# Kernel optimization log

Measured on AMD Instinct MI355X. Metric: run time of the kernel, lower is better.

## Reference

```python
import jax, jax.numpy as jnp
import numpy as np

B, D, R = 16384, 4096, 64       # batch tokens, embed_dim, low_rank_dimension
N_PART = 8                       # number of subspace partitions
P = R // N_PART                  # partition size = 8
N_SEL = 4                        # partitions selected per example


def setup_inputs() -> dict:
    key = jax.random.key(0)
    k1, k2, k3, k4 = jax.random.split(key, 4)
    base = jax.random.normal(k1, (B, D), dtype=jnp.float32)
    source = jax.random.normal(k2, (B, D), dtype=jnp.float32)
    # orthogonal low-rank rotation (torch.nn.utils.parametrizations.orthogonal)
    W, _ = jnp.linalg.qr(jax.random.normal(k3, (D, R), dtype=jnp.float32))  # [D, R], orthonormal cols
    subspaces = jax.random.randint(k4, (B, N_SEL), 0, N_PART)               # partition ids per example
    return {"base": base, "source": source, "W": W, "subspaces": subspaces}


def reference(base, source, W, subspaces):
    # rotate into low-rank space: [B, R]
    rotated_base = base @ W
    rotated_source = source @ W
    diff = rotated_source - rotated_base

    # per-example selected rotated-space indices (contiguous partitions of size P)
    # idx[b] = concat over selected partitions of [p*P, p*P+P)
    idx = (subspaces[:, :, None] * P + jnp.arange(P)).reshape(B, N_SEL * P)  # [B, N_SEL*P]

    # Selecting columns of diff and matching rows of W.T, then matmul, is
    # equivalent to masking unselected rotated dims to zero and doing one GEMM.
    mask = jnp.zeros((B, R), dtype=diff.dtype).at[jnp.arange(B)[:, None], idx].set(1.0)
    output = base + (diff * mask) @ W.T  # [B, D]
    return output.astype(base.dtype)
```

## Files before the change

### kernel.cpp

```cpp
#include <hip/hip_runtime.h>


#define D_DIM 4096
#define R_DIM 64
#define BM    16
#define KC    64
#define KW    1024

typedef short bf16vec8 __attribute__((ext_vector_type(8)));
typedef float f32x4v  __attribute__((ext_vector_type(4)));

#define OFF_STAGE   0
#define OFF_SCRATCH 8192
#define OFF_RM      26624
#define SMEM_BYTES  28672

__device__ __forceinline__ unsigned int f2bf_u(float f) {
  unsigned int u = __builtin_bit_cast(unsigned int, f);
  return (u + 0x7fffu + ((u >> 16) & 1u)) >> 16;
}
__device__ __forceinline__ unsigned int pack2bf(float a, float b) {
  return f2bf_u(a) | (f2bf_u(b) << 16);
}
__device__ __forceinline__ float bfbits2f(unsigned short s) {
  unsigned int u = ((unsigned int)s) << 16;
  return __builtin_bit_cast(float, u);
}

__global__ __launch_bounds__(256)
void lrri_prep(const float* __restrict__ W, unsigned short* __restrict__ Wt,
               unsigned short* __restrict__ Wb) {
  const int idx = blockIdx.x * blockDim.x + threadIdx.x;
  const int k = idx >> 4;
  const int j = (idx & 15) * 4;
  float4 w = *(const float4*)(W + (size_t)k * R_DIM + j);
  ushort4 p;
  p.x = (unsigned short)f2bf_u(w.x);
  p.y = (unsigned short)f2bf_u(w.y);
  p.z = (unsigned short)f2bf_u(w.z);
  p.w = (unsigned short)f2bf_u(w.w);
  *(ushort4*)(Wb + (size_t)k * R_DIM + j) = p;
  Wt[(size_t)(j + 0) * D_DIM + k] = p.x;
  Wt[(size_t)(j + 1) * D_DIM + k] = p.y;
  Wt[(size_t)(j + 2) * D_DIM + k] = p.z;
  Wt[(size_t)(j + 3) * D_DIM + k] = p.w;
}

template<bool USE_WS>
__global__ __launch_bounds__(256, 4)
void lrri_fused(const float* __restrict__ base, const float* __restrict__ srcp,
                const float* __restrict__ W, const int* __restrict__ subs,
                const unsigned short* __restrict__ Wt_bf,
                const unsigned short* __restrict__ Wb_bf,
                float* __restrict__ out)
{
  __shared__ __align__(16) unsigned char smem[SMEM_BYTES];
  const int tid  = threadIdx.x;
  const int wave = tid >> 6;
  const int lane = tid & 63;
  const int l4   = lane & 15;
  const int g    = lane >> 4;
  const long rowbase = (long)blockIdx.x * BM;

  unsigned short* stage = (unsigned short*)(smem + OFF_STAGE + wave * 2048);

  f32x4v acc[4];
  #pragma unroll
  for (int t = 0; t < 4; ++t) acc[t] = (f32x4v){0.f, 0.f, 0.f, 0.f};

  const int kw0 = wave * KW;
  #pragma unroll 1
  for (int c = 0; c < KW / KC; ++c) {
    const int kbase = kw0 + c * KC;
    float4 b4[4], s4[4];
    #pragma unroll
    for (int i = 0; i < 4; ++i) {
      const int r = g + i * 4;
      const long off = (rowbase + r) * D_DIM + kbase + l4 * 4;
      b4[i] = *(const float4*)(base + off);
      s4[i] = *(const float4*)(srcp + off);
    }
    #pragma unroll
    for (int i = 0; i < 4; ++i) {
      const int r = g + i * 4;
      uint2 dp;
      dp.x = pack2bf(s4[i].x - b4[i].x, s4[i].y - b4[i].y);
      dp.y = pack2bf(s4[i].z - b4[i].z, s4[i].w - b4[i].w);
      *(uint2*)((unsigned char*)stage + r * 128 + l4 * 8) = dp;
    }
    uint4 af[2];
    #pragma unroll
    for (int s = 0; s < 2; ++s)
      af[s] = *(const uint4*)((unsigned char*)stage + l4 * 128 + s * 64 + g * 16);
    #pragma unroll
    for (int t = 0; t < 4; ++t) {
      #pragma unroll
      for (int s = 0; s < 2; ++s) {
        uint4 bfrag;
        if (USE_WS) {
          bfrag = *(const uint4*)(Wt_bf + (size_t)(t * 16 + l4) * D_DIM +
                                  kbase + s * 32 + g * 8);
        } else {
          unsigned int p[4];
          #pragma unroll
          for (int e2 = 0; e2 < 4; ++e2) {
            float wa = W[(size_t)(kbase + s * 32 + g * 8 + e2 * 2    ) * R_DIM + t * 16 + l4];
            float wb = W[(size_t)(kbase + s * 32 + g * 8 + e2 * 2 + 1) * R_DIM + t * 16 + l4];
            p[e2] = pack2bf(wa, wb);
          }
          bfrag.x = p[0]; bfrag.y = p[1]; bfrag.z = p[2]; bfrag.w = p[3];
        }
        acc[t] = __builtin_amdgcn_mfma_f32_16x16x32_bf16(
            __builtin_bit_cast(bf16vec8, af[s]),
            __builtin_bit_cast(bf16vec8, bfrag), acc[t], 0, 0, 0);
      }
    }
  }
  {
    float* part = (float*)(smem + OFF_SCRATCH + wave * 4608);
    #pragma unroll
    for (int t = 0; t < 4; ++t)
      #pragma unroll
      for (int i = 0; i < 4; ++i)
        part[(g * 4 + i) * 72 + t * 16 + l4] = acc[t][i];
  }
  __syncthreads();

  {
    const int row = tid >> 4, jg = tid & 15;
    const float* p0 = (const float*)(smem + OFF_SCRATCH);
    int4 sb = *(const int4*)(subs + (rowbase + row) * 4);
    unsigned mbits = (1u << sb.x) | (1u << sb.y) | (1u << sb.z) | (1u << sb.w);
    unsigned short vals[4];
    #pragma unroll
    for (int jj = 0; jj < 4; ++jj) {
      const int j = jg * 4 + jj;
      float sum = p0[row * 72 + j] + p0[1152 + row * 72 + j] +
                  p0[2304 + row * 72 + j] + p0[3456 + row * 72 + j];
      vals[jj] = ((mbits >> (j >> 3)) & 1u) ? (unsigned short)f2bf_u(sum)
                                            : (unsigned short)0;
    }
    unsigned short* rm = (unsigned short*)(smem + OFF_RM);
    uint2 pk;
    pk.x = (unsigned)vals[0] | ((unsigned)vals[1] << 16);
    pk.y = (unsigned)vals[2] | ((unsigned)vals[3] << 16);
    *(uint2*)(rm + row * 64 + jg * 4) = pk;
  }
  __syncthreads();

  uint4 a2[2];
  {
    const unsigned short* rm = (const unsigned short*)(smem + OFF_RM);
    #pragma unroll
    for (int s = 0; s < 2; ++s)
      a2[s] = *(const uint4*)((const unsigned char*)rm + l4 * 128 + s * 64 + g * 16);
  }
  float* cbuf = (float*)(smem + OFF_SCRATCH + wave * 4608);
  #pragma unroll 1
  for (int grp = 0; grp < 16; ++grp) {
    const int cbase = wave * 1024 + grp * 64;
    float4 bb[4];
    #pragma unroll
    for (int s2 = 0; s2 < 4; ++s2) {
      const int r = g + s2 * 4;
      bb[s2] = *(const float4*)(base + (rowbase + r) * D_DIM + cbase + l4 * 4);
    }
    #pragma unroll
    for (int t = 0; t < 4; ++t) {
      f32x4v a = (f32x4v){0.f, 0.f, 0.f, 0.f};
      #pragma unroll
      for (int s = 0; s < 2; ++s) {
        uint4 bfrag;
        if (USE_WS) {
          bfrag = *(const uint4*)(Wb_bf + (size_t)(cbase + t * 16 + l4) * R_DIM +
                                  s * 32 + g * 8);
        } else {
          const float* wp = W + (size_t)(cbase + t * 16 + l4) * R_DIM + s * 32 + g * 8;
          float4 wa = *(const float4*)(wp);
          float4 wb = *(const float4*)(wp + 4);
          bfrag.x = pack2bf(wa.x, wa.y); bfrag.y = pack2bf(wa.z, wa.w);
          bfrag.z = pack2bf(wb.x, wb.y); bfrag.w = pack2bf(wb.z, wb.w);
        }
        a = __builtin_amdgcn_mfma_f32_16x16x32_bf16(
            __builtin_bit_cast(bf16vec8, a2[s]),
            __builtin_bit_cast(bf16vec8, bfrag), a, 0, 0, 0);
      }
      #pragma unroll
      for (int i = 0; i < 4; ++i)
        cbuf[(g * 4 + i) * 72 + t * 16 + l4] = a[i];
    }
    #pragma unroll
    for (int s2 = 0; s2 < 4; ++s2) {
      const int r = g + s2 * 4;
      f32x4v cv = *(const f32x4v*)(cbuf + r * 72 + l4 * 4);
      float4 o;
      o.x = cv[0] + bb[s2].x;
      o.y = cv[1] + bb[s2].y;
      o.z = cv[2] + bb[s2].z;
      o.w = cv[3] + bb[s2].w;
      *(float4*)(out + (rowbase + r) * D_DIM + cbase + l4 * 4) = o;
    }
  }
}

extern "C" void kernel_launch(void* const* d_in, const int* in_sizes, int n_in,
                              void* d_out, int out_size, void* d_ws, size_t ws_size,
                              hipStream_t stream) {
  const float* base = (const float*)d_in[0];
  const float* srcp = (const float*)d_in[1];
  const float* W    = (const float*)d_in[2];
  const int*   subs = (const int*)d_in[3];
  float* out = (float*)d_out;

  const int nblocks = 16384 / BM;
  const size_t wbytes = (size_t)2 * R_DIM * D_DIM * sizeof(unsigned short);
  if (d_ws && ws_size >= wbytes) {
    unsigned short* Wt = (unsigned short*)d_ws;
    unsigned short* Wb = Wt + (size_t)R_DIM * D_DIM;
    lrri_prep<<<256, 256, 0, stream>>>(W, Wt, Wb);
    lrri_fused<true><<<nblocks, 256, 0, stream>>>(base, srcp, W, subs, Wt, Wb, out);
  } else {
    lrri_fused<false><<<nblocks, 256, 0, stream>>>(base, srcp, W, subs, nullptr, nullptr, out);
  }
}
```

Before: 262.0 us.

## Load A fragments directly into registers, fully unroll loops, double-buffer epilogue scratch

The first GEMM phase now loads base and source in the MFMA A-fragment layout: each lane reads row l4 at its own k offsets and packs bf16 in registers. This removes the per-chunk LDS stage write and read-back. Both main loops are fully unrolled, and the per-wave epilogue scratch alternates between two halves so consecutive groups do not reuse the same LDS buffer. The changes raise register and shared-memory use (38.9KB per block), which could reduce occupancy. The new global load pattern reads two 16-byte segments per row per lane instead of fully coalesced row segments.

```diff
diff --git a/kernel.cpp b/kernel.cpp
--- a/kernel.cpp
+++ b/kernel.cpp
@@ -10,10 +10,9 @@
 typedef short bf16vec8 __attribute__((ext_vector_type(8)));
 typedef float f32x4v  __attribute__((ext_vector_type(4)));
 
-#define OFF_STAGE   0
-#define OFF_SCRATCH 8192
-#define OFF_RM      26624
-#define SMEM_BYTES  28672
+#define WAVE_SCR_F  2304
+#define OFF_RM      36864
+#define SMEM_BYTES  38912
 
 __device__ __forceinline__ unsigned int f2bf_u(float f) {
   unsigned int u = __builtin_bit_cast(unsigned int, f);
@@ -21,10 +20,6 @@
 }
 __device__ __forceinline__ unsigned int pack2bf(float a, float b) {
   return f2bf_u(a) | (f2bf_u(b) << 16);
-}
-__device__ __forceinline__ float bfbits2f(unsigned short s) {
-  unsigned int u = ((unsigned int)s) << 16;
-  return __builtin_bit_cast(float, u);
 }
 
 __global__ __launch_bounds__(256)
@@ -62,36 +57,35 @@
   const int g    = lane >> 4;
   const long rowbase = (long)blockIdx.x * BM;
 
-  unsigned short* stage = (unsigned short*)(smem + OFF_STAGE + wave * 2048);
-
   f32x4v acc[4];
   #pragma unroll
   for (int t = 0; t < 4; ++t) acc[t] = (f32x4v){0.f, 0.f, 0.f, 0.f};
 
-  const int kw0 = wave * KW;
-  #pragma unroll 1
+  const int  kw0  = wave * KW;
+  const long arow = (rowbase + l4) * D_DIM;
+
+  #pragma unroll
   for (int c = 0; c < KW / KC; ++c) {
     const int kbase = kw0 + c * KC;
-    float4 b4[4], s4[4];
-    #pragma unroll
-    for (int i = 0; i < 4; ++i) {
-      const int r = g + i * 4;
-      const long off = (rowbase + r) * D_DIM + kbase + l4 * 4;
-      b4[i] = *(const float4*)(base + off);
-      s4[i] = *(const float4*)(srcp + off);
-    }
-    #pragma unroll
-    for (int i = 0; i < 4; ++i) {
-      const int r = g + i * 4;
-      uint2 dp;
-      dp.x = pack2bf(s4[i].x - b4[i].x, s4[i].y - b4[i].y);
-      dp.y = pack2bf(s4[i].z - b4[i].z, s4[i].w - b4[i].w);
-      *(uint2*)((unsigned char*)stage + r * 128 + l4 * 8) = dp;
+    float4 vb[4], vs[4];
+    #pragma unroll
+    for (int q = 0; q < 4; ++q) {
+      const long off = arow + kbase + (q >> 1) * 32 + g * 8 + (q & 1) * 4;
+      vb[q] = *(const float4*)(base + off);
+      vs[q] = *(const float4*)(srcp + off);
     }
     uint4 af[2];
     #pragma unroll
-    for (int s = 0; s < 2; ++s)
-      af[s] = *(const uint4*)((unsigned char*)stage + l4 * 128 + s * 64 + g * 16);
+    for (int s = 0; s < 2; ++s) {
+      float d0 = vs[s*2].x - vb[s*2].x, d1 = vs[s*2].y - vb[s*2].y;
+      float d2 = vs[s*2].z - vb[s*2].z, d3 = vs[s*2].w - vb[s*2].w;
+      float d4 = vs[s*2+1].x - vb[s*2+1].x, d5 = vs[s*2+1].y - vb[s*2+1].y;
+      float d6 = vs[s*2+1].z - vb[s*2+1].z, d7 = vs[s*2+1].w - vb[s*2+1].w;
+      af[s].x = pack2bf(d0, d1);
+      af[s].y = pack2bf(d2, d3);
+      af[s].z = pack2bf(d4, d5);
+      af[s].w = pack2bf(d6, d7);
+    }
     #pragma unroll
     for (int t = 0; t < 4; ++t) {
       #pragma unroll
@@ -117,7 +111,7 @@
     }
   }
   {
-    float* part = (float*)(smem + OFF_SCRATCH + wave * 4608);
+    float* part = (float*)smem + wave * WAVE_SCR_F;
     #pragma unroll
     for (int t = 0; t < 4; ++t)
       #pragma unroll
@@ -128,15 +122,16 @@
 
   {
     const int row = tid >> 4, jg = tid & 15;
-    const float* p0 = (const float*)(smem + OFF_SCRATCH);
+    const float* p0 = (const float*)smem;
     int4 sb = *(const int4*)(subs + (rowbase + row) * 4);
     unsigned mbits = (1u << sb.x) | (1u << sb.y) | (1u << sb.z) | (1u << sb.w);
     unsigned short vals[4];
     #pragma unroll
     for (int jj = 0; jj < 4; ++jj) {
       const int j = jg * 4 + jj;
-      float sum = p0[row * 72 + j] + p0[1152 + row * 72 + j] +
-                  p0[2304 + row * 72 + j] + p0[3456 + row * 72 + j];
+      float sum = p0[row * 72 + j] + p0[WAVE_SCR_F + row * 72 + j] +
+                  p0[2 * WAVE_SCR_F + row * 72 + j] +
+                  p0[3 * WAVE_SCR_F + row * 72 + j];
       vals[jj] = ((mbits >> (j >> 3)) & 1u) ? (unsigned short)f2bf_u(sum)
                                             : (unsigned short)0;
     }
@@ -150,13 +145,13 @@
 
   uint4 a2[2];
   {
-    const unsigned short* rm = (const unsigned short*)(smem + OFF_RM);
+    const unsigned char* rm = smem + OFF_RM;
     #pragma unroll
     for (int s = 0; s < 2; ++s)
-      a2[s] = *(const uint4*)((const unsigned char*)rm + l4 * 128 + s * 64 + g * 16);
-  }
-  float* cbuf = (float*)(smem + OFF_SCRATCH + wave * 4608);
-  #pragma unroll 1
+      a2[s] = *(const uint4*)(rm + l4 * 128 + s * 64 + g * 16);
+  }
+  float* cb = (float*)smem + wave * WAVE_SCR_F;
+  #pragma unroll
   for (int grp = 0; grp < 16; ++grp) {
     const int cbase = wave * 1024 + grp * 64;
     float4 bb[4];
@@ -165,6 +160,7 @@
       const int r = g + s2 * 4;
       bb[s2] = *(const float4*)(base + (rowbase + r) * D_DIM + cbase + l4 * 4);
     }
+    float* cbuf = cb + (grp & 1) * 1152;
     #pragma unroll
     for (int t = 0; t < 4; ++t) {
       f32x4v a = (f32x4v){0.f, 0.f, 0.f, 0.f};
```

Result: slower. 285.4 us (+8.9%).

## Double-buffer base/source tiles via async global-to-LDS loads with swizzle

Applied to the files above, without the earlier changes.

Replaces per-wave direct register loads of base/source with double-buffered global_load_lds staging into a swizzled 64KB LDS buffer, and prefetches W fragments via inline asm one stage ahead so memory overlaps MFMA work. Column chunks are now shared across all waves per stage, with per-block rotated starting offsets to spread DRAM/L2 traffic. The epilogue writes full 256-column rows per wave for wider coalesced stores. Increasing LDS to ~66KB lowers occupancy (launch bounds 4→2), and the added barriers could offset the overlap gains.

```diff
diff --git a/kernel.cpp b/kernel.cpp
--- a/kernel.cpp
+++ b/kernel.cpp
@@ -4,16 +4,31 @@
 #define D_DIM 4096
 #define R_DIM 64
 #define BM    16
-#define KC    64
-#define KW    1024
+#define NSC   16
 
 typedef short bf16vec8 __attribute__((ext_vector_type(8)));
 typedef float f32x4v  __attribute__((ext_vector_type(4)));
-
-#define OFF_STAGE   0
-#define OFF_SCRATCH 8192
-#define OFF_RM      26624
-#define SMEM_BYTES  28672
+typedef unsigned int u32x4 __attribute__((ext_vector_type(4)));
+
+#define BUFSZ       32768
+#define OFF_RM      65536
+#define SMEM_BYTES  67840
+
+#define VMWAIT(N)                                              \
+  do {                                                         \
+    asm volatile("s_waitcnt vmcnt(" #N ")" ::: "memory");      \
+    __builtin_amdgcn_sched_barrier(0);                         \
+  } while (0)
+#define LGKM0()                                                \
+  do {                                                         \
+    asm volatile("s_waitcnt lgkmcnt(0)" ::: "memory");         \
+    __builtin_amdgcn_sched_barrier(0);                         \
+  } while (0)
+#define BAR()                                                  \
+  do {                                                         \
+    __builtin_amdgcn_s_barrier();                              \
+    __builtin_amdgcn_sched_barrier(0);                         \
+  } while (0)
 
 __device__ __forceinline__ unsigned int f2bf_u(float f) {
   unsigned int u = __builtin_bit_cast(unsigned int, f);
@@ -22,9 +37,10 @@
 __device__ __forceinline__ unsigned int pack2bf(float a, float b) {
   return f2bf_u(a) | (f2bf_u(b) << 16);
 }
-__device__ __forceinline__ float bfbits2f(unsigned short s) {
-  unsigned int u = ((unsigned int)s) << 16;
-  return __builtin_bit_cast(float, u);
+__device__ __forceinline__ void async_ld16(const void* gp, void* lp) {
+  __builtin_amdgcn_global_load_lds(
+      (const __attribute__((address_space(1))) void*)gp,
+      (__attribute__((address_space(3))) void*)lp, 16, 0, 0);
 }
 
 __global__ __launch_bounds__(256)
@@ -47,7 +63,7 @@
 }
 
 template<bool USE_WS>
-__global__ __launch_bounds__(256, 4)
+__global__ __launch_bounds__(256, 2)
 void lrri_fused(const float* __restrict__ base, const float* __restrict__ srcp,
                 const float* __restrict__ W, const int* __restrict__ subs,
                 const unsigned short* __restrict__ Wt_bf,
@@ -61,63 +77,130 @@
   const int l4   = lane & 15;
   const int g    = lane >> 4;
   const long rowbase = (long)blockIdx.x * BM;
-
-  unsigned short* stage = (unsigned short*)(smem + OFF_STAGE + wave * 2048);
+  const int off1 = (blockIdx.x * 7) & 15;
+  const int off2 = (blockIdx.x * 5) & 15;
+
+  auto stage = [&](int i) {
+    const int sc = (i + off1) & 15;
+    unsigned char* buf = smem + (i & 1) * BUFSZ;
+    const unsigned lb = (unsigned)(lane * 16);
+    #pragma unroll
+    for (int q = 0; q < 4; ++q) {
+      const int r = wave * 4 + q;
+      const unsigned sw = (unsigned)((r & 7) << 4);
+      const long goff = (rowbase + r) * (long)D_DIM + sc * 256 + ((lb ^ sw) >> 2);
+      async_ld16(base + goff, buf + r * 1024);
+      async_ld16(srcp + goff, buf + 16384 + r * 1024);
+    }
+  };
+
+  auto wload = [&](u32x4 (&dst)[8], int kb) {
+    const char* wbp = (const char*)Wt_bf + (size_t)kb * 2 + l4 * 8192 + g * 16;
+    const char* a0 = wbp;
+    const char* a1 = wbp + 16 * 8192;
+    const char* a2 = wbp + 32 * 8192;
+    const char* a3 = wbp + 48 * 8192;
+    asm volatile(
+        "global_load_dwordx4 %0, %8, off\n\t"
+        "global_load_dwordx4 %1, %8, off offset:64\n\t"
+        "global_load_dwordx4 %2, %9, off\n\t"
+        "global_load_dwordx4 %3, %9, off offset:64\n\t"
+        "global_load_dwordx4 %4, %10, off\n\t"
+        "global_load_dwordx4 %5, %10, off offset:64\n\t"
+        "global_load_dwordx4 %6, %11, off\n\t"
+        "global_load_dwordx4 %7, %11, off offset:64"
+        : "=&v"(dst[0]), "=&v"(dst[1]), "=&v"(dst[2]), "=&v"(dst[3]),
+          "=&v"(dst[4]), "=&v"(dst[5]), "=&v"(dst[6]), "=&v"(dst[7])
+        : "v"(a0), "v"(a1), "v"(a2), "v"(a3)
+        : "memory");
+  };
 
   f32x4v acc[4];
   #pragma unroll
   for (int t = 0; t < 4; ++t) acc[t] = (f32x4v){0.f, 0.f, 0.f, 0.f};
 
-  const int kw0 = wave * KW;
-  #pragma unroll 1
-  for (int c = 0; c < KW / KC; ++c) {
-    const int kbase = kw0 + c * KC;
-    float4 b4[4], s4[4];
-    #pragma unroll
-    for (int i = 0; i < 4; ++i) {
-      const int r = g + i * 4;
-      const long off = (rowbase + r) * D_DIM + kbase + l4 * 4;
-      b4[i] = *(const float4*)(base + off);
-      s4[i] = *(const float4*)(srcp + off);
-    }
-    #pragma unroll
-    for (int i = 0; i < 4; ++i) {
-      const int r = g + i * 4;
-      uint2 dp;
-      dp.x = pack2bf(s4[i].x - b4[i].x, s4[i].y - b4[i].y);
-      dp.y = pack2bf(s4[i].z - b4[i].z, s4[i].w - b4[i].w);
-      *(uint2*)((unsigned char*)stage + r * 128 + l4 * 8) = dp;
-    }
-    uint4 af[2];
-    #pragma unroll
-    for (int s = 0; s < 2; ++s)
-      af[s] = *(const uint4*)((unsigned char*)stage + l4 * 128 + s * 64 + g * 16);
-    #pragma unroll
-    for (int t = 0; t < 4; ++t) {
-      #pragma unroll
-      for (int s = 0; s < 2; ++s) {
-        uint4 bfrag;
-        if (USE_WS) {
-          bfrag = *(const uint4*)(Wt_bf + (size_t)(t * 16 + l4) * D_DIM +
-                                  kbase + s * 32 + g * 8);
-        } else {
-          unsigned int p[4];
-          #pragma unroll
-          for (int e2 = 0; e2 < 4; ++e2) {
-            float wa = W[(size_t)(kbase + s * 32 + g * 8 + e2 * 2    ) * R_DIM + t * 16 + l4];
-            float wb = W[(size_t)(kbase + s * 32 + g * 8 + e2 * 2 + 1) * R_DIM + t * 16 + l4];
-            p[e2] = pack2bf(wa, wb);
-          }
-          bfrag.x = p[0]; bfrag.y = p[1]; bfrag.z = p[2]; bfrag.w = p[3];
-        }
+  const int kq = wave * 64;
+
+  auto compute = [&](int i, const u32x4 (&wf)[8]) {
+    const unsigned char* buf = smem + (i & 1) * BUFSZ;
+    const unsigned sw = (unsigned)((l4 & 7) << 4);
+    u32x4 af[2];
+    #pragma unroll
+    for (int s = 0; s < 2; ++s) {
+      const unsigned cB = (unsigned)(wave * 256 + s * 128 + g * 32);
+      const unsigned cb0 = cB ^ sw, cb1 = (cB + 16) ^ sw;
+      float4 fb0 = *(const float4*)(buf + l4 * 1024 + cb0);
+      float4 fb1 = *(const float4*)(buf + l4 * 1024 + cb1);
+      float4 fs0 = *(const float4*)(buf + 16384 + l4 * 1024 + cb0);
+      float4 fs1 = *(const float4*)(buf + 16384 + l4 * 1024 + cb1);
+      af[s].x = pack2bf(fs0.x - fb0.x, fs0.y - fb0.y);
+      af[s].y = pack2bf(fs0.z - fb0.z, fs0.w - fb0.w);
+      af[s].z = pack2bf(fs1.x - fb1.x, fs1.y - fb1.y);
+      af[s].w = pack2bf(fs1.z - fb1.z, fs1.w - fb1.w);
+    }
+    #pragma unroll
+    for (int t = 0; t < 4; ++t)
+      #pragma unroll
+      for (int s = 0; s < 2; ++s)
         acc[t] = __builtin_amdgcn_mfma_f32_16x16x32_bf16(
             __builtin_bit_cast(bf16vec8, af[s]),
-            __builtin_bit_cast(bf16vec8, bfrag), acc[t], 0, 0, 0);
+            __builtin_bit_cast(bf16vec8, wf[t * 2 + s]), acc[t], 0, 0, 0);
+  };
+
+  auto kb_of = [&](int i) { return ((i + off1) & 15) * 256 + kq; };
+
+  if constexpr (USE_WS) {
+    u32x4 wbA[8], wbB[8];
+    stage(0); wload(wbA, kb_of(0));
+    #pragma unroll 1
+    for (int i = 0; i < 14; i += 2) {
+      LGKM0(); BAR();
+      stage(i + 1); wload(wbB, kb_of(i + 1));
+      VMWAIT(16);
+      BAR();
+      compute(i, wbA);
+      LGKM0(); BAR();
+      stage(i + 2); wload(wbA, kb_of(i + 2));
+      VMWAIT(16);
+      BAR();
+      compute(i + 1, wbB);
+    }
+    LGKM0(); BAR();
+    stage(15); wload(wbB, kb_of(15));
+    VMWAIT(16);
+    BAR();
+    compute(14, wbA);
+    LGKM0(); BAR();
+    VMWAIT(0);
+    BAR();
+    compute(15, wbB);
+  } else {
+    #pragma unroll 1
+    for (int i = 0; i < NSC; ++i) {
+      LGKM0(); BAR();
+      stage(i);
+      VMWAIT(0);
+      BAR();
+      const int kb = kb_of(i);
+      u32x4 wf[8];
+      #pragma unroll
+      for (int ts = 0; ts < 8; ++ts) {
+        const int t = ts >> 1, s = ts & 1;
+        unsigned int pq[4];
+        #pragma unroll
+        for (int e2 = 0; e2 < 4; ++e2) {
+          float wa = W[(size_t)(kb + s * 32 + g * 8 + e2 * 2    ) * R_DIM + t * 16 + l4];
+          float wb = W[(size_t)(kb + s * 32 + g * 8 + e2 * 2 + 1) * R_DIM + t * 16 + l4];
+          pq[e2] = pack2bf(wa, wb);
+        }
+        wf[ts].x = pq[0]; wf[ts].y = pq[1]; wf[ts].z = pq[2]; wf[ts].w = pq[3];
       }
-    }
-  }
+      compute(i, wf);
+    }
+  }
+
   {
-    float* part = (float*)(smem + OFF_SCRATCH + wave * 4608);
+    float* part = (float*)(smem + wave * 4608);
     #pragma unroll
     for (int t = 0; t < 4; ++t)
       #pragma unroll
@@ -128,7 +211,7 @@
 
   {
     const int row = tid >> 4, jg = tid & 15;
-    const float* p0 = (const float*)(smem + OFF_SCRATCH);
+    const float* p0 = (const float*)smem;
     int4 sb = *(const int4*)(subs + (rowbase + row) * 4);
     unsigned mbits = (1u << sb.x) | (1u << sb.y) | (1u << sb.z) | (1u << sb.w);
     unsigned short vals[4];
@@ -144,27 +227,20 @@
     uint2 pk;
     pk.x = (unsigned)vals[0] | ((unsigned)vals[1] << 16);
     pk.y = (unsigned)vals[2] | ((unsigned)vals[3] << 16);
-    *(uint2*)(rm + row * 64 + jg * 4) = pk;
+    *(uint2*)(rm + row * 72 + jg * 4) = pk;
   }
   __syncthreads();
 
   uint4 a2[2];
-  {
-    const unsigned short* rm = (const unsigned short*)(smem + OFF_RM);
-    #pragma unroll
-    for (int s = 0; s < 2; ++s)
-      a2[s] = *(const uint4*)((const unsigned char*)rm + l4 * 128 + s * 64 + g * 16);
-  }
-  float* cbuf = (float*)(smem + OFF_SCRATCH + wave * 4608);
+  #pragma unroll
+  for (int s = 0; s < 2; ++s)
+    a2[s] = *(const uint4*)(smem + OFF_RM + l4 * 144 + s * 64 + g * 16);
+
   #pragma unroll 1
-  for (int grp = 0; grp < 16; ++grp) {
-    const int cbase = wave * 1024 + grp * 64;
-    float4 bb[4];
-    #pragma unroll
-    for (int s2 = 0; s2 < 4; ++s2) {
-      const int r = g + s2 * 4;
-      bb[s2] = *(const float4*)(base + (rowbase + r) * D_DIM + cbase + l4 * 4);
-    }
+  for (int i2 = 0; i2 < NSC; ++i2) {
+    const int sc2 = (i2 + off2) & 15;
+    const int cb = sc2 * 256;
+    float* cbuf = (float*)(smem + (i2 & 1) * 16384);
     #pragma unroll
     for (int t = 0; t < 4; ++t) {
       f32x4v a = (f32x4v){0.f, 0.f, 0.f, 0.f};
@@ -172,14 +248,15 @@
       for (int s = 0; s < 2; ++s) {
         uint4 bfrag;
         if (USE_WS) {
-          bfrag = *(const uint4*)(Wb_bf + (size_t)(cbase + t * 16 + l4) * R_DIM +
-                                  s * 32 + g * 8);
+          bfrag = *(const uint4*)(Wb_bf +
+              (size_t)(cb + wave * 64 + t * 16 + l4) * R_DIM + s * 32 + g * 8);
         } else {
-          const float* wp = W + (size_t)(cbase + t * 16 + l4) * R_DIM + s * 32 + g * 8;
+          const float* wp = W + (size_t)(cb + wave * 64 + t * 16 + l4) * R_DIM +
+                            s * 32 + g * 8;
           float4 wa = *(const float4*)(wp);
-          float4 wb = *(const float4*)(wp + 4);
+          float4 wc = *(const float4*)(wp + 4);
           bfrag.x = pack2bf(wa.x, wa.y); bfrag.y = pack2bf(wa.z, wa.w);
-          bfrag.z = pack2bf(wb.x, wb.y); bfrag.w = pack2bf(wb.z, wb.w);
+          bfrag.z = pack2bf(wc.x, wc.y); bfrag.w = pack2bf(wc.z, wc.w);
         }
         a = __builtin_amdgcn_mfma_f32_16x16x32_bf16(
             __builtin_bit_cast(bf16vec8, a2[s]),
@@ -187,18 +264,21 @@
       }
       #pragma unroll
       for (int i = 0; i < 4; ++i)
-        cbuf[(g * 4 + i) * 72 + t * 16 + l4] = a[i];
-    }
-    #pragma unroll
-    for (int s2 = 0; s2 < 4; ++s2) {
-      const int r = g + s2 * 4;
-      f32x4v cv = *(const f32x4v*)(cbuf + r * 72 + l4 * 4);
+        cbuf[(g * 4 + i) * 256 + wave * 64 + t * 16 + l4] = a[i];
+    }
+    __syncthreads();
+    #pragma unroll
+    for (int q = 0; q < 4; ++q) {
+      const int r = wave * 4 + q;
+      const long go = (rowbase + r) * (long)D_DIM + cb + lane * 4;
+      f32x4v cv = *(const f32x4v*)(cbuf + r * 256 + lane * 4);
+      float4 bb = *(const float4*)(base + go);
       float4 o;
-      o.x = cv[0] + bb[s2].x;
-      o.y = cv[1] + bb[s2].y;
-      o.z = cv[2] + bb[s2].z;
-      o.w = cv[3] + bb[s2].w;
-      *(float4*)(out + (rowbase + r) * D_DIM + cbase + l4 * 4) = o;
+      o.x = cv[0] + bb.x;
+      o.y = cv[1] + bb.y;
+      o.z = cv[2] + bb.z;
+      o.w = cv[3] + bb.w;
+      *(float4*)(out + go) = o;
     }
   }
 }
```

Result: faster. 243.7 us (-7.0%).
